# Kernel optimization log

Hardware: AMD Instinct MI355X
Metric: run time of the kernel (lower is better)

Reference implementation:

```python
import jax, jax.numpy as jnp
import numpy as np

ALPHA = 0.1

def setup_inputs() -> dict:
    key = jax.random.key(0)
    x = jax.random.normal(key, (8, 8192, 512), dtype=jnp.float32)
    return {"x": x}

def reference(x) -> jnp.ndarray:
    # EMA recurrence: y_0 = x_0; y_t = alpha*x_t + (1-alpha)*y_{t-1}
    # x: [B, T, F] -> scan over T with carry [B, F]
    alpha = jnp.asarray(ALPHA, dtype=x.dtype)
    xt = jnp.swapaxes(x, 0, 1)  # [T, B, F]

    def step(prev, curr):
        smoothed = alpha * curr + (1 - alpha) * prev
        return smoothed, smoothed

    y0 = xt[0]
    _, ys = jax.lax.scan(step, y0, xt[1:])  # ys: [T-1, B, F]
    out = jnp.concatenate([y0[None], ys], axis=0)  # [T, B, F]
    return jnp.swapaxes(out, 0, 1)  # [B, T, F]
```

## Files before the change

### kernel.cpp

```cpp
#include <hip/hip_runtime.h>


constexpr int   B_    = 8;
constexpr int   T_    = 8192;
constexpr int   F_    = 512;
constexpr int   CHUNK = 256;
constexpr int   HALO  = 192;
constexpr float ALPHA = 0.1f;
constexpr float DECAY = 0.9f;

__global__ __launch_bounds__(256, 4)
void ema_chunked_kernel(const float* __restrict__ x, float* __restrict__ y) {
    const int f     = blockIdx.x * 256 + threadIdx.x;
    const int chunk = blockIdx.y;
    const int b     = blockIdx.z;

    const int t0 = chunk * CHUNK;
    const size_t base = (size_t)b * T_ * F_ + f;

    float s = 0.0f;
    int tstart = t0;

    if (chunk == 0) {
        s = x[base];
        y[base] = s;
        tstart = 1;
    } else {
        const float* p = x + base + (size_t)(t0 - HALO) * F_;
        #pragma unroll 8
        for (int i = 0; i < HALO; ++i) {
            s = fmaf(DECAY, s, ALPHA * p[0]);
            p += F_;
        }
    }

    const float* p = x + base + (size_t)tstart * F_;
    float*       q = y + base + (size_t)tstart * F_;
    const int n = t0 + CHUNK - tstart;
    #pragma unroll 8
    for (int i = 0; i < n; ++i) {
        s = fmaf(DECAY, s, ALPHA * p[0]);
        q[0] = s;
        p += F_;
        q += F_;
    }
}

extern "C" void kernel_launch(void* const* d_in, const int* in_sizes, int n_in,
                              void* d_out, int out_size, void* d_ws, size_t ws_size,
                              hipStream_t stream) {
    const float* x = (const float*)d_in[0];
    float* y = (float*)d_out;

    dim3 grid(F_ / 256, T_ / CHUNK, B_);
    dim3 block(256);
    ema_chunked_kernel<<<grid, block, 0, stream>>>(x, y);
}
```

Before: 57.57 us.

## Vectorize EMA scan with float2 and shrink chunk and halo lengths

Each thread now processes two adjacent features via float2 loads and stores, and time chunks shrink to 64 with a 96-step halo, doubling the block count. This shortens each thread's serial dependency chain and raises parallelism for a latency-bound recurrence. In exchange, redundant halo reads grow relative to useful work and the truncation error from the shorter halo rises. Early chunks get an exact prefix path instead.

```diff
diff --git a/kernel.cpp b/kernel.cpp
--- a/kernel.cpp
+++ b/kernel.cpp
@@ -4,55 +4,74 @@
 constexpr int   B_    = 8;
 constexpr int   T_    = 8192;
 constexpr int   F_    = 512;
-constexpr int   CHUNK = 256;
-constexpr int   HALO  = 192;
+constexpr int   F2    = F_ / 2;
+constexpr int   CHUNK = 64;
+constexpr int   HALO  = 96;
 constexpr float ALPHA = 0.1f;
 constexpr float DECAY = 0.9f;
 
-__global__ __launch_bounds__(256, 4)
-void ema_chunked_kernel(const float* __restrict__ x, float* __restrict__ y) {
-    const int f     = blockIdx.x * 256 + threadIdx.x;
-    const int chunk = blockIdx.y;
-    const int b     = blockIdx.z;
+__global__ __launch_bounds__(256, 8)
+void ema_chunked_f2_kernel(const float2* __restrict__ xv, float2* __restrict__ yv) {
+    const int tid   = threadIdx.x;
+    const int chunk = blockIdx.x;
+    const int b     = blockIdx.y;
 
     const int t0 = chunk * CHUNK;
-    const size_t base = (size_t)b * T_ * F_ + f;
+    const size_t base = (size_t)b * T_ * F2 + tid;
 
-    float s = 0.0f;
-    int tstart = t0;
+    float s0 = 0.0f, s1 = 0.0f;
+    int tstart;
 
     if (chunk == 0) {
-        s = x[base];
-        y[base] = s;
+        float2 v = xv[base];
+        s0 = v.x; s1 = v.y;
+        yv[base] = v;
         tstart = 1;
+    } else if (t0 <= HALO) {
+        float2 v = xv[base];
+        s0 = v.x; s1 = v.y;
+        const float2* p = xv + base + (size_t)1 * F2;
+        for (int t = 1; t < t0; ++t) {
+            float2 u = p[0];
+            s0 = fmaf(DECAY, s0, ALPHA * u.x);
+            s1 = fmaf(DECAY, s1, ALPHA * u.y);
+            p += F2;
+        }
+        tstart = t0;
     } else {
-        const float* p = x + base + (size_t)(t0 - HALO) * F_;
+        const float2* p = xv + base + (size_t)(t0 - HALO) * F2;
         #pragma unroll 8
         for (int i = 0; i < HALO; ++i) {
-            s = fmaf(DECAY, s, ALPHA * p[0]);
-            p += F_;
+            float2 v = p[0];
+            s0 = fmaf(DECAY, s0, ALPHA * v.x);
+            s1 = fmaf(DECAY, s1, ALPHA * v.y);
+            p += F2;
         }
+        tstart = t0;
     }
 
-    const float* p = x + base + (size_t)tstart * F_;
-    float*       q = y + base + (size_t)tstart * F_;
+    const float2* p = xv + base + (size_t)tstart * F2;
+    float2*       q = yv + base + (size_t)tstart * F2;
     const int n = t0 + CHUNK - tstart;
     #pragma unroll 8
     for (int i = 0; i < n; ++i) {
-        s = fmaf(DECAY, s, ALPHA * p[0]);
-        q[0] = s;
-        p += F_;
-        q += F_;
+        float2 v = p[0];
+        s0 = fmaf(DECAY, s0, ALPHA * v.x);
+        s1 = fmaf(DECAY, s1, ALPHA * v.y);
+        float2 w; w.x = s0; w.y = s1;
+        q[0] = w;
+        p += F2;
+        q += F2;
     }
 }
 
 extern "C" void kernel_launch(void* const* d_in, const int* in_sizes, int n_in,
                               void* d_out, int out_size, void* d_ws, size_t ws_size,
                               hipStream_t stream) {
-    const float* x = (const float*)d_in[0];
-    float* y = (float*)d_out;
+    const float2* xv = (const float2*)d_in[0];
+    float2* yv = (float2*)d_out;
 
-    dim3 grid(F_ / 256, T_ / CHUNK, B_);
+    dim3 grid(T_ / CHUNK, B_);
     dim3 block(256);
-    ema_chunked_kernel<<<grid, block, 0, stream>>>(x, y);
+    ema_chunked_f2_kernel<<<grid, block, 0, stream>>>(xv, yv);
 }
```

Result: slower. 74.06 us (+28.6%).
